# Performance work log

Measured on AMD Instinct MI355X. Metric: run time of the kernel, lower is better.

The kernel has to match this reference:

```python
import jax, jax.numpy as jnp
import numpy as np

N_WIRES = 9
N_QRAM_LAYERS = 3
N_QCLS_LAYERS = 5

X = jnp.array([[0, 1], [1, 0]], dtype=jnp.complex64)
CNOT = jnp.array([[1, 0, 0, 0], [0, 1, 0, 0], [0, 0, 0, 1], [0, 0, 1, 0]], dtype=jnp.complex64)


def _rx(t):
    c = jnp.cos(t / 2)
    s = jnp.sin(t / 2)
    # works for scalar t -> (2,2) or batched t [B] -> (B,2,2)
    return jnp.stack([jnp.stack([c + 0j, -1j * s], -1), jnp.stack([-1j * s, c + 0j], -1)], -2)


def _ry(t):
    c = jnp.cos(t / 2)
    s = jnp.sin(t / 2)
    return jnp.stack([jnp.stack([c, -s], -1), jnp.stack([s, c], -1)], -2).astype(jnp.complex64)


def _rz(t):
    e = jnp.exp(-0.5j * t)
    f = jnp.exp(0.5j * t)
    z = jnp.zeros_like(e)
    return jnp.stack([jnp.stack([e, z], -1), jnp.stack([z, f], -1)], -2)


def _rot(phi, theta, omega):
    # PennyLane Rot(phi, theta, omega) = RZ(omega) @ RY(theta) @ RZ(phi)
    return _rz(omega) @ _ry(theta) @ _rz(phi)


def _crz(t):
    e = jnp.exp(-0.5j * t)
    f = jnp.exp(0.5j * t)
    one = jnp.ones((), e.dtype)
    return jnp.diag(jnp.stack([one, one, e, f]))


def _crx(t):
    return jnp.eye(4, dtype=jnp.complex64).at[2:, 2:].set(_rx(t))


def apply_1q(state, U, w):
    # state: [B] + (2,)*N_WIRES ; wire w -> axis 1+w
    s = jnp.moveaxis(state, 1 + w, -1)
    if U.ndim == 3:  # per-sample gate (embedding)
        s = jnp.einsum('bij,b...j->b...i', U, s)
    else:
        s = jnp.einsum('ij,...j->...i', U, s)
    return jnp.moveaxis(s, -1, 1 + w)


def apply_2q(state, U, c, t):
    s = jnp.moveaxis(state, (1 + c, 1 + t), (-2, -1))
    shp = s.shape
    s = s.reshape(shp[:-2] + (4,))
    s = jnp.einsum('ij,...j->...i', U, s)
    return jnp.moveaxis(s.reshape(shp), (-2, -1), (1 + c, 1 + t))


def embed(state, adds):
    # AngleEmbedding: RX(adds[:, i]) on wire i
    for i in range(N_WIRES):
        state = apply_1q(state, _rx(adds[:, i]), i)
    return state


def entangle_block(state, p):
    # p: [36] = 4 params per wire-pair step
    j = 0
    for i in range(N_WIRES):
        ip = (i + 1) % N_WIRES
        state = apply_1q(state, _ry(p[j]), i)
        state = apply_1q(state, _ry(p[j + 1]), ip)
        state = apply_2q(state, CNOT, i, ip)
        state = apply_2q(state, _crz(p[j + 2]), i, ip)
        state = apply_1q(state, X, ip)
        state = apply_2q(state, _crx(p[j + 3]), i, ip)
        j += 4
    return state


def sel_layer(state, w, r):
    # one StronglyEntanglingLayers layer: Rot on each wire, then CNOT ring of range r
    for i in range(N_WIRES):
        state = apply_1q(state, _rot(w[i, 0], w[i, 1], w[i, 2]), i)
    for i in range(N_WIRES):
        state = apply_2q(state, CNOT, i, (i + r) % N_WIRES)
    return state


def circuit(adds, params, weights, params2):
    B = adds.shape[0]
    state = jnp.zeros((B,) + (2,) * N_WIRES, jnp.complex64)
    state = state.at[(slice(None),) + (0,) * N_WIRES].set(1.0)
    state = embed(state, adds)
    for l in range(N_QRAM_LAYERS):
        state = entangle_block(state, params[l * 36:(l + 1) * 36])
    for l in range(N_QRAM_LAYERS):
        r = (l % (N_WIRES - 1)) + 1  # PennyLane default ranges
        state = sel_layer(state, weights[l], r)
    for l in range(N_QCLS_LAYERS):
        state = entangle_block(state, params2[l * 36:(l + 1) * 36])
    probs = jnp.abs(state) ** 2
    p = probs.reshape(B, 2, -1).sum(-1)  # marginal over wire 0
    return p[:, 0] - p[:, 1]  # <PauliZ(0)>


def setup_inputs() -> dict:
    key = jax.random.key(0)
    k1, k2, k3, k4 = jax.random.split(key, 4)
    B = 8192
    return {
        'adds': jax.random.normal(k1, (B, N_WIRES), dtype=jnp.float32),
        'params': jax.random.normal(k2, (N_QRAM_LAYERS * 36,), dtype=jnp.float32),
        'weights': jax.random.normal(k3, (N_QRAM_LAYERS, N_WIRES, N_QRAM_LAYERS), dtype=jnp.float32),
        'params2': jax.random.normal(k4, (N_QCLS_LAYERS * 36,), dtype=jnp.float32),
    }


def reference(adds, params, weights, params2):
    return circuit(adds, params, weights, params2)
```

## Files before the change

### kernel.cpp

```cpp
#include <hip/hip_runtime.h>

#define NQ 9
#define NS 512
#define M2 1024
#define NSIMB 512

#define ENT_H_BASE 0
#define ROT_BASE   1024
#define ROT3_BASE  1240
#define M0123_BASE 1624
#define M78_BASE   5720
#define COEF_FLOATS 6744

typedef __attribute__((ext_vector_type(8))) short bf16x8;
typedef __attribute__((ext_vector_type(4))) float f32x4;

__device__ inline unsigned short f2bf(float f){
  unsigned int u = __float_as_uint(f);
  u += 0x7fffu + ((u >> 16) & 1u);
  return (unsigned short)(u >> 16);
}


template<int LM>
__device__ inline float lxor(float v){
  if constexpr (LM == 1)
    return __int_as_float(__builtin_amdgcn_mov_dpp(__float_as_int(v), 0xB1, 0xF, 0xF, true));
  else if constexpr (LM == 2)
    return __int_as_float(__builtin_amdgcn_mov_dpp(__float_as_int(v), 0x4E, 0xF, 0xF, true));
  else if constexpr (LM == 3)
    return __int_as_float(__builtin_amdgcn_mov_dpp(__float_as_int(v), 0x1B, 0xF, 0xF, true));
  else if constexpr (LM < 32)
    return __int_as_float(__builtin_amdgcn_ds_swizzle(__float_as_int(v), (LM<<10)|0x1F));
  else
    return __shfl_xor(v, LM);
}

template<int CM, int TM>
__device__ inline void step_swz(float& ax, float& ay, int lane, const float* g){
  float tx = lxor<TM>(ax),      ty = lxor<TM>(ay);
  float cx = lxor<CM>(ax),      cy = lxor<CM>(ay);
  float bx = lxor<(CM^TM)>(ax), by = lxor<(CM^TM)>(ay);
  int p = ((lane & CM) ? 2 : 0) | ((lane & TM) ? 1 : 0);
  float4 hx = *(const float4*)(g + p*4);
  float4 hy = *(const float4*)(g + 16 + p*4);
  float ox = ax, oy = ay;
  ax = hx.x*ox - hy.x*oy + hx.y*tx - hy.y*ty
     + hx.z*cx - hy.z*cy + hx.w*bx - hy.w*by;
  ay = hx.x*oy + hy.x*ox + hx.y*ty + hy.y*tx
     + hx.z*cy + hy.z*cx + hx.w*by + hy.w*bx;
}

__device__ inline void mrg16(float& ax, float& ay, int i, float2* xb, const float* Mt){
  xb[i] = make_float2(ax, ay);
  __syncthreads();
  int p = (i >> 5) & 15;
  const float* Mr = Mt + p*32;
  int base = i & 31;
  float s0x=0.f,s0y=0.f,s1x=0.f,s1y=0.f;
  #pragma unroll
  for (int q = 0; q < 16; q += 2){
    float2 v0 = xb[(q<<5)|base];
    float2 v1 = xb[((q+1)<<5)|base];
    float m0x = Mr[q*2],   m0y = Mr[q*2+1];
    float m1x = Mr[q*2+2], m1y = Mr[q*2+3];
    s0x += m0x*v0.x - m0y*v0.y;  s0y += m0x*v0.y + m0y*v0.x;
    s1x += m1x*v1.x - m1y*v1.y;  s1y += m1x*v1.y + m1y*v1.x;
  }
  ax = s0x + s1x; ay = s0y + s1y;
}

__device__ inline void mrg8_78(float& ax, float& ay, int i, float2* xb, const float* Mt){
  xb[i] = make_float2(ax, ay);
  __syncthreads();
  int p = (((i>>1)&1)<<2) | ((i&1)<<1) | ((i>>8)&1);
  const float* Mr = Mt + p*16;
  int ib = i & 0x0FC;
  float s0x=0.f,s0y=0.f,s1x=0.f,s1y=0.f;
  #pragma unroll
  for (int q = 0; q < 8; q += 2){
    int j0 = ib | ((q>>2)<<1) | ((q>>1)&1);
    float2 v0 = xb[j0];
    float2 v1 = xb[j0 | 0x100];
    float m0x = Mr[q*2],   m0y = Mr[q*2+1];
    float m1x = Mr[q*2+2], m1y = Mr[q*2+3];
    s0x += m0x*v0.x - m0y*v0.y;  s0y += m0x*v0.y + m0y*v0.x;
    s1x += m1x*v1.x - m1y*v1.y;  s1y += m1x*v1.y + m1y*v1.x;
  }
  ax = s0x + s1x; ay = s0y + s1y;
}

__device__ inline void rot3R(float& ax, float& ay, int i, float2* xb, const float* Mt){
  xb[i] = make_float2(ax, ay);
  __syncthreads();
  int p = i >> 6;
  const float* Mr = Mt + p*16;
  int base = i & 63;
  float s0x=0.f,s0y=0.f,s1x=0.f,s1y=0.f;
  #pragma unroll
  for (int q = 0; q < 8; q += 2){
    float2 v0 = xb[(q<<6)|base];
    float2 v1 = xb[((q+1)<<6)|base];
    float m0x = Mr[q*2],   m0y = Mr[q*2+1];
    float m1x = Mr[q*2+2], m1y = Mr[q*2+3];
    s0x += m0x*v0.x - m0y*v0.y;  s0y += m0x*v0.y + m0y*v0.x;
    s1x += m1x*v1.x - m1y*v1.y;  s1y += m1x*v1.y + m1y*v1.x;
  }
  ax = s0x + s1x; ay = s0y + s1y;
}

template<int LM>
__device__ inline void rot_swz(float& ax, float& ay, int lane, const float* u){
  float px = lxor<LM>(ax), py = lxor<LM>(ay);
  float4 uu = *(const float4*)(u + ((lane & LM) ? 4 : 0));
  float nx = uu.x*ax - uu.y*ay + uu.z*px - uu.w*py;
  float ny = uu.x*ay + uu.y*ax + uu.z*py + uu.w*px;
  ax = nx; ay = ny;
}

template<int I = 3>
__device__ inline void sel_lane_rots(float& ax, float& ay, int lane, const float* ub){
  rot_swz<(1<<(8-I))>(ax, ay, lane, ub + I*8);
  if constexpr (I < 8) sel_lane_rots<I+1>(ax, ay, lane, ub);
}

__device__ inline void ring_rt(float& ax, float& ay, int i, float2* buf, int R){
  buf[i] = make_float2(ax, ay);
  __syncthreads();
  int s = i;
  for (int k = 8; k >= 0; --k){
    int bc = 8 - k;
    int it = k + R; if (it >= 9) it -= 9;
    int bt = 8 - it;
    s ^= ((s >> bc) & 1) << bt;
  }
  float2 v = buf[s];
  ax = v.x; ay = v.y;
}

__device__ inline void entM(float& ax, float& ay, int i, int lane,
                            float2* bA, float2* bB, const float* scoef, int blk){
  mrg16(ax, ay, i, bA, scoef + M0123_BASE + blk*512);
  step_swz<32,16>(ax, ay, lane, scoef + ENT_H_BASE + (blk*4+0)*32);
  step_swz<16, 8>(ax, ay, lane, scoef + ENT_H_BASE + (blk*4+1)*32);
  step_swz< 8, 4>(ax, ay, lane, scoef + ENT_H_BASE + (blk*4+2)*32);
  step_swz< 4, 2>(ax, ay, lane, scoef + ENT_H_BASE + (blk*4+3)*32);
  mrg8_78(ax, ay, i, bB, scoef + M78_BASE + blk*128);
}


__global__ __launch_bounds__(512) void sim_prep(const float* __restrict__ params,
                                                const float* __restrict__ weights,
                                                const float* __restrict__ params2,
                                                const float* __restrict__ adds,
                                                unsigned short* __restrict__ A2,
                                                unsigned short* __restrict__ cT,
                                                float* __restrict__ out, int B){
  int tid = threadIdx.x;

  if (blockIdx.x >= NSIMB){
    int gid = (blockIdx.x - NSIMB) * 512 + tid;
    int b = gid >> 6;
    int lane = gid & 63;
    if (b < B){
      const float* ab = adds + b * NQ;
      float cw[NQ], sw[NQ];
      #pragma unroll
      for (int w = 0; w < NQ; ++w)
        __sincosf(0.5f * ab[w], &sw[w], &cw[w]);
      float p6 = 1.f;
      #pragma unroll
      for (int w = 0; w < 6; ++w)
        p6 *= ((lane >> (5 - w)) & 1) ? sw[w] : cw[w];
      union { unsigned short u[8]; uint4 v; } pk;
      #pragma unroll
      for (int j = 0; j < 8; ++j){
        float p = p6 * (((j>>2)&1) ? sw[6] : cw[6])
                     * (((j>>1)&1) ? sw[7] : cw[7])
                     * (( j    &1) ? sw[8] : cw[8]);
        pk.u[j] = f2bf(p);
      }
      *(uint4*)(cT + (size_t)b * NS + lane*8) = pk.v;
    }
    if (gid < B) out[gid] = 0.f;
    return;
  }

  __shared__ float2 ebuf[1024];
  __shared__ float scoef[COEF_FLOATS];
  float2* ebufA = ebuf;
  float2* ebufB = ebuf + 512;
  float* graw = (float*)ebuf;

  if (tid < 72){
    int blk = tid / 9, I = tid % 9;
    const float* p = (blk < 3) ? params + blk*36 : params2 + (blk-3)*36;
    float s0,c0,s1,c1,s2,c2,s3,c3;
    __sincosf(0.5f*p[4*I+0], &s0, &c0);
    __sincosf(0.5f*p[4*I+1], &s1, &c1);
    __sincosf(0.5f*p[4*I+2], &s2, &c2);
    __sincosf(0.5f*p[4*I+3], &s3, &c3);
    float m[4][4] = {
      { c0*c1, -c0*s1, -s0*c1,  s0*s1},
      { c0*s1,  c0*c1, -s0*s1, -s0*c1},
      { s0*c1, -s0*s1,  c0*c1, -c0*s1},
      { s0*s1,  s0*c1,  c0*s1,  c0*c1}};
    float gx[4][4], gy[4][4];
    #pragma unroll
    for (int q = 0; q < 4; ++q){
      gx[0][q] = m[1][q];  gy[0][q] = 0.f;
      gx[1][q] = m[0][q];  gy[1][q] = 0.f;
      gx[2][q] =  c3*c2*m[2][q] - s3*s2*m[3][q];
      gy[2][q] =  c3*s2*m[2][q] - s3*c2*m[3][q];
      gx[3][q] =  s3*s2*m[2][q] + c3*c2*m[3][q];
      gy[3][q] = -(s3*c2*m[2][q] + c3*s2*m[3][q]);
    }
    if (I >= 3 && I <= 6){
      float* dst = scoef + ENT_H_BASE + (blk*4 + (I-3))*32;
      #pragma unroll
      for (int pp = 0; pp < 4; ++pp)
        #pragma unroll
        for (int d = 0; d < 4; ++d){
          dst[pp*4+d]    = gx[pp][pp^d];
          dst[16+pp*4+d] = gy[pp][pp^d];
        }
    } else {
      float* dst = (I < 3) ? graw + (blk*3 + I)*32
                           : graw + 768 + (blk*2 + (I-7))*32;
      #pragma unroll
      for (int pp = 0; pp < 4; ++pp)
        #pragma unroll
        for (int q = 0; q < 4; ++q){
          dst[(pp*4+q)*2]   = gx[pp][q];
          dst[(pp*4+q)*2+1] = gy[pp][q];
        }
    }
  } else if (tid < 99){
    int r = tid - 72;
    int l = r / 9, i = r % 9;
    const float* w = weights + l*27 + 3*i;
    float phi = w[0], th = w[1], om = w[2];
    float sT,cT,sA,cA,sB,cB;
    __sincosf(0.5f*th, &sT, &cT);
    __sincosf(0.5f*(phi+om), &sA, &cA);
    __sincosf(0.5f*(om-phi), &sB, &cB);
    float* dst = scoef + ROT_BASE + r*8;
    dst[0] =  cA*cT;  dst[1] = -sA*cT;
    dst[2] = -cB*sT;  dst[3] =  sB*sT;
    dst[4] =  cA*cT;  dst[5] =  sA*cT;
    dst[6] =  cB*sT;  dst[7] =  sB*sT;
  } else if (tid < 123){
    int idx = tid - 99;
    int l = idx >> 3, p = idx & 7;
    float e0x[3], e0y[3], e1x[3], e1y[3];
    #pragma unroll
    for (int w = 0; w < 3; ++w){
      const float* wp = weights + l*27 + 3*w;
      float phi = wp[0], th = wp[1], om = wp[2];
      float sT,cT,sA,cA,sB,cB;
      __sincosf(0.5f*th, &sT, &cT);
      __sincosf(0.5f*(phi+om), &sA, &cA);
      __sincosf(0.5f*(om-phi), &sB, &cB);
      int pw = (p >> (2 - w)) & 1;
      if (pw == 0){ e0x[w] =  cA*cT; e0y[w] = -sA*cT; e1x[w] = -cB*sT; e1y[w] =  sB*sT; }
      else        { e0x[w] =  cB*sT; e0y[w] =  sB*sT; e1x[w] =  cA*cT; e1y[w] =  sA*cT; }
    }
    float* dst = scoef + ROT3_BASE + l*128 + p*16;
    #pragma unroll
    for (int q = 0; q < 8; ++q){
      float rx = 1.f, ry = 0.f;
      #pragma unroll
      for (int w = 0; w < 3; ++w){
        int qw = (q >> (2 - w)) & 1;
        float fx = qw ? e1x[w] : e0x[w];
        float fy = qw ? e1y[w] : e0y[w];
        float nx = rx*fx - ry*fy;
        float ny = rx*fy + ry*fx;
        rx = nx; ry = ny;
      }
      dst[q*2]   = rx;
      dst[q*2+1] = ry;
    }
  }
  __syncthreads();

  {
    int blk = tid >> 6;
    const float* G0 = graw + (blk*3+0)*32;
    const float* G1 = graw + (blk*3+1)*32;
    const float* G2 = graw + (blk*3+2)*32;
    int e4 = (tid & 63) * 4;
    #pragma unroll
    for (int k = 0; k < 4; ++k){
      int e = e4 + k;
      int p = e >> 4, q = e & 15;
      int a=(p>>3)&1, b=(p>>2)&1, c=(p>>1)&1, d=p&1;
      int ee=(q>>3)&1, f=(q>>2)&1, g=(q>>1)&1, h=q&1;
      float sx = 0.f, sy = 0.f;
      #pragma unroll
      for (int m = 0; m < 2; ++m)
        #pragma unroll
        for (int n = 0; n < 2; ++n){
          const float* z2 = G2 + ((c*2+d)*4 + (n*2+h))*2;
          const float* z1 = G1 + ((b*2+n)*4 + (m*2+g))*2;
          const float* z0 = G0 + ((a*2+m)*4 + (ee*2+f))*2;
          float ux = z2[0]*z1[0] - z2[1]*z1[1];
          float uy = z2[0]*z1[1] + z2[1]*z1[0];
          float vx = ux*z0[0] - uy*z0[1];
          float vy = ux*z0[1] + uy*z0[0];
          sx += vx; sy += vy;
        }
      scoef[M0123_BASE + blk*512 + (p*16+q)*2]   = sx;
      scoef[M0123_BASE + blk*512 + (p*16+q)*2+1] = sy;
    }
    const float* G7 = graw + 768 + (blk*2+0)*32;
    const float* G8 = graw + 768 + (blk*2+1)*32;
    int e = tid & 63;
    int p = e >> 3, q = e & 7;
    int a=(p>>2)&1, b=(p>>1)&1, c=p&1;
    int d=(q>>2)&1, ei=(q>>1)&1, f=q&1;
    float sx = 0.f, sy = 0.f;
    #pragma unroll
    for (int m = 0; m < 2; ++m){
      const float* z8 = G8 + ((b*2+c)*4 + (m*2+f))*2;
      const float* z7 = G7 + ((a*2+m)*4 + (d*2+ei))*2;
      sx += z8[0]*z7[0] - z8[1]*z7[1];
      sy += z8[0]*z7[1] + z8[1]*z7[0];
    }
    scoef[M78_BASE + blk*128 + (p*8+q)*2]   = sx;
    scoef[M78_BASE + blk*128 + (p*8+q)*2+1] = sy;
  }
  __syncthreads();

  int i = tid, lane = tid & 63;
  int col = blockIdx.x;
  float ax, ay;
  int pc = __popc((unsigned)col) & 3;
  float prx = (pc==0) ? 1.f : (pc==2 ? -1.f : 0.f);
  float pry = (pc==3) ? 1.f : (pc==1 ? -1.f : 0.f);
  ax = (i == col) ? prx : 0.f;
  ay = (i == col) ? pry : 0.f;

  #pragma unroll 1
  for (int blk = 0; blk < 3; ++blk)
    entM(ax, ay, i, lane, ebufA, ebufB, scoef, blk);
  #pragma unroll 1
  for (int L = 0; L < 3; ++L){
    rot3R(ax, ay, i, ebufA, scoef + ROT3_BASE + L*128);
    sel_lane_rots<3>(ax, ay, lane, scoef + ROT_BASE + L*72);
    ring_rt(ax, ay, i, ebufB, L + 1);
  }
  #pragma unroll 1
  for (int blk = 3; blk < 8; ++blk)
    entM(ax, ay, i, lane, ebufA, ebufB, scoef, blk);

  int c = col >> 3, sub = col & 7;
  size_t base = (size_t)c * 1024;
  A2[(base + i)*8 + sub]       = f2bf(ax);
  A2[(base + 512 + i)*8 + sub] = f2bf(ay);
}

__global__ __launch_bounds__(256) void gemm_out(const unsigned short* __restrict__ A2,
                                                const unsigned short* __restrict__ cT,
                                                float* __restrict__ out){
  int bx = blockIdx.x;
  int by = blockIdx.y;
  int tid = threadIdx.x;
  int wave = tid >> 6, lane = tid & 63;
  int wy = wave >> 1, wx = wave & 1;
  int lane15 = lane & 15, quad = lane >> 4;
  int rowBase = by*128 + wy*64;
  int colBase = bx*128 + wx*64;
  const bf16x8* Ap8 = (const bf16x8*)A2;
  const short* Bp = (const short*)cT;

  f32x4 acc[4][4];
  #pragma unroll
  for (int i = 0; i < 4; ++i)
    #pragma unroll
    for (int j = 0; j < 4; ++j)
      acc[i][j] = (f32x4){0.f, 0.f, 0.f, 0.f};

  #pragma unroll 4
  for (int k0 = 0; k0 < NS; k0 += 32){
    bf16x8 a[4], b[4];
    int c = (k0 >> 3) + quad;
    #pragma unroll
    for (int mi = 0; mi < 4; ++mi)
      a[mi] = Ap8[(size_t)c*1024 + rowBase + mi*16 + lane15];
    #pragma unroll
    for (int ni = 0; ni < 4; ++ni)
      b[ni] = *(const bf16x8*)(Bp + (size_t)(colBase + ni*16 + lane15)*NS + k0 + quad*8);
    #pragma unroll
    for (int mi = 0; mi < 4; ++mi)
      #pragma unroll
      for (int ni = 0; ni < 4; ++ni)
        acc[mi][ni] = __builtin_amdgcn_mfma_f32_16x16x32_bf16(a[mi], b[ni], acc[mi][ni], 0, 0, 0);
  }

  float sign = (by & 2) ? -1.f : 1.f;
  #pragma unroll
  for (int ni = 0; ni < 4; ++ni){
    float cs = 0.f;
    #pragma unroll
    for (int mi = 0; mi < 4; ++mi)
      #pragma unroll
      for (int r = 0; r < 4; ++r)
        cs += acc[mi][ni][r] * acc[mi][ni][r];
    cs += __shfl_xor(cs, 16);
    cs += __shfl_xor(cs, 32);
    if (quad == 0)
      atomicAdd(out + colBase + ni*16 + lane15, sign * cs);
  }
}

extern "C" void kernel_launch(void* const* d_in, const int* in_sizes, int n_in,
                              void* d_out, int out_size, void* d_ws, size_t ws_size,
                              hipStream_t stream) {
  const float* adds    = (const float*)d_in[0];
  const float* params  = (const float*)d_in[1];
  const float* weights = (const float*)d_in[2];
  const float* params2 = (const float*)d_in[3];
  float* out = (float*)d_out;
  int B = in_sizes[0] / NQ;

  unsigned short* A2 = (unsigned short*)d_ws;
  unsigned short* cT = A2 + (size_t)M2 * NS;

  int prepBlocks = (B * 64 + 511) / 512;
  hipLaunchKernelGGL(sim_prep, dim3(NSIMB + prepBlocks), dim3(512), 0, stream,
                     params, weights, params2, adds, A2, cT, out, B);
  hipLaunchKernelGGL(gemm_out, dim3(B / 128, 8), dim3(256), 0, stream, A2, cT, out);
}
```

Measured before the change: 113.8 us.

## Fuse selector layer rotations into 16x16 merged matrices and permute-on-write

The selector layers' 3-wire rotation matmul and the first lane rotation are now precomputed into a single 16x16 complex matrix per layer, applied with the existing mrg16 routine. The ring CNOT permutation is folded into the shared-memory write index through a precomputed lookup table, which removes a separate store/sync/load pass per layer. The GEMM kernel is also changed to 512 threads with 8 waves, each computing a 64x32 tile, which halves per-wave accumulator registers. The fused step does more multiply-adds per element, and shared memory usage grows.

```diff
diff --git a/kernel.cpp b/kernel.cpp
--- a/kernel.cpp
+++ b/kernel.cpp
@@ -8,9 +8,10 @@
 #define ENT_H_BASE 0
 #define ROT_BASE   1024
 #define ROT3_BASE  1240
-#define M0123_BASE 1624
-#define M78_BASE   5720
-#define COEF_FLOATS 6744
+#define ROT16_BASE 1624
+#define M0123_BASE 3160
+#define M78_BASE   7256
+#define COEF_FLOATS 8280
 
 typedef __attribute__((ext_vector_type(8))) short bf16x8;
 typedef __attribute__((ext_vector_type(4))) float f32x4;
@@ -51,8 +52,9 @@
      + hx.z*cy + hy.z*cx + hx.w*by + hy.w*bx;
 }
 
-__device__ inline void mrg16(float& ax, float& ay, int i, float2* xb, const float* Mt){
-  xb[i] = make_float2(ax, ay);
+__device__ inline void mrg16(float& ax, float& ay, int i, int wi, float2* xb,
+                             const float* Mt){
+  xb[wi] = make_float2(ax, ay);
   __syncthreads();
   int p = (i >> 5) & 15;
   const float* Mr = Mt + p*32;
@@ -90,25 +92,6 @@
   ax = s0x + s1x; ay = s0y + s1y;
 }
 
-__device__ inline void rot3R(float& ax, float& ay, int i, float2* xb, const float* Mt){
-  xb[i] = make_float2(ax, ay);
-  __syncthreads();
-  int p = i >> 6;
-  const float* Mr = Mt + p*16;
-  int base = i & 63;
-  float s0x=0.f,s0y=0.f,s1x=0.f,s1y=0.f;
-  #pragma unroll
-  for (int q = 0; q < 8; q += 2){
-    float2 v0 = xb[(q<<6)|base];
-    float2 v1 = xb[((q+1)<<6)|base];
-    float m0x = Mr[q*2],   m0y = Mr[q*2+1];
-    float m1x = Mr[q*2+2], m1y = Mr[q*2+3];
-    s0x += m0x*v0.x - m0y*v0.y;  s0y += m0x*v0.y + m0y*v0.x;
-    s1x += m1x*v1.x - m1y*v1.y;  s1y += m1x*v1.y + m1y*v1.x;
-  }
-  ax = s0x + s1x; ay = s0y + s1y;
-}
-
 template<int LM>
 __device__ inline void rot_swz(float& ax, float& ay, int lane, const float* u){
   float px = lxor<LM>(ax), py = lxor<LM>(ay);
@@ -118,34 +101,20 @@
   ax = nx; ay = ny;
 }
 
-template<int I = 3>
+template<int I = 4>
 __device__ inline void sel_lane_rots(float& ax, float& ay, int lane, const float* ub){
   rot_swz<(1<<(8-I))>(ax, ay, lane, ub + I*8);
   if constexpr (I < 8) sel_lane_rots<I+1>(ax, ay, lane, ub);
 }
 
-__device__ inline void ring_rt(float& ax, float& ay, int i, float2* buf, int R){
-  buf[i] = make_float2(ax, ay);
-  __syncthreads();
-  int s = i;
-  for (int k = 8; k >= 0; --k){
-    int bc = 8 - k;
-    int it = k + R; if (it >= 9) it -= 9;
-    int bt = 8 - it;
-    s ^= ((s >> bc) & 1) << bt;
-  }
-  float2 v = buf[s];
-  ax = v.x; ay = v.y;
-}
-
-__device__ inline void entM(float& ax, float& ay, int i, int lane,
-                            float2* bA, float2* bB, const float* scoef, int blk){
-  mrg16(ax, ay, i, bA, scoef + M0123_BASE + blk*512);
+__device__ inline void entM(float& ax, float& ay, int i, int wi, int lane,
+                            float2* bX, float2* bY, const float* scoef, int blk){
+  mrg16(ax, ay, i, wi, bX, scoef + M0123_BASE + blk*512);
   step_swz<32,16>(ax, ay, lane, scoef + ENT_H_BASE + (blk*4+0)*32);
   step_swz<16, 8>(ax, ay, lane, scoef + ENT_H_BASE + (blk*4+1)*32);
   step_swz< 8, 4>(ax, ay, lane, scoef + ENT_H_BASE + (blk*4+2)*32);
   step_swz< 4, 2>(ax, ay, lane, scoef + ENT_H_BASE + (blk*4+3)*32);
-  mrg8_78(ax, ay, i, bB, scoef + M78_BASE + blk*128);
+  mrg8_78(ax, ay, i, bY, scoef + M78_BASE + blk*128);
 }
 
 
@@ -188,6 +157,7 @@
 
   __shared__ float2 ebuf[1024];
   __shared__ float scoef[COEF_FLOATS];
+  __shared__ unsigned short slut[3][512];
   float2* ebufA = ebuf;
   float2* ebufB = ebuf + 512;
   float* graw = (float*)ebuf;
@@ -329,11 +299,37 @@
     }
     scoef[M78_BASE + blk*128 + (p*8+q)*2]   = sx;
     scoef[M78_BASE + blk*128 + (p*8+q)*2+1] = sy;
+
+    for (int e2 = tid; e2 < 768; e2 += 512){
+      int l = e2 >> 8, pq = e2 & 255;
+      int pp = pq >> 4, qq = pq & 15;
+      const float* R3 = scoef + ROT3_BASE + l*128 + (pp>>1)*16 + (qq>>1)*2;
+      const float* U = scoef + ROT_BASE + (l*9+3)*8;
+      int pb = pp & 1, qb = qq & 1;
+      float ux, uy;
+      if (pb == 0){ if (qb == 0){ ux=U[0]; uy=U[1]; } else { ux=U[2]; uy=U[3]; } }
+      else        { if (qb == 1){ ux=U[4]; uy=U[5]; } else { ux=U[6]; uy=U[7]; } }
+      float rx = R3[0], ry = R3[1];
+      scoef[ROT16_BASE + l*512 + pp*32 + qq*2]   = rx*ux - ry*uy;
+      scoef[ROT16_BASE + l*512 + pp*32 + qq*2+1] = rx*uy + ry*ux;
+    }
+
+    for (int R = 1; R <= 3; ++R){
+      int s = tid;
+      for (int k = 8; k >= 0; --k){
+        int bc = 8 - k;
+        int it = k + R; if (it >= 9) it -= 9;
+        int bt = 8 - it;
+        s ^= ((s >> bc) & 1) << bt;
+      }
+      slut[R-1][s] = (unsigned short)tid;
+    }
   }
   __syncthreads();
 
   int i = tid, lane = tid & 63;
   int col = blockIdx.x;
+  int w1 = slut[0][i], w2 = slut[1][i], w3 = slut[2][i];
   float ax, ay;
   int pc = __popc((unsigned)col) & 3;
   float prx = (pc==0) ? 1.f : (pc==2 ? -1.f : 0.f);
@@ -343,16 +339,19 @@
 
   #pragma unroll 1
   for (int blk = 0; blk < 3; ++blk)
-    entM(ax, ay, i, lane, ebufA, ebufB, scoef, blk);
+    entM(ax, ay, i, i, lane, ebufA, ebufB, scoef, blk);
+
+  mrg16(ax, ay, i, i,  ebufA, scoef + ROT16_BASE + 0*512);
+  sel_lane_rots<4>(ax, ay, lane, scoef + ROT_BASE + 0*72);
+  mrg16(ax, ay, i, w1, ebufB, scoef + ROT16_BASE + 1*512);
+  sel_lane_rots<4>(ax, ay, lane, scoef + ROT_BASE + 1*72);
+  mrg16(ax, ay, i, w2, ebufA, scoef + ROT16_BASE + 2*512);
+  sel_lane_rots<4>(ax, ay, lane, scoef + ROT_BASE + 2*72);
+
+  entM(ax, ay, i, w3, lane, ebufB, ebufA, scoef, 3);
   #pragma unroll 1
-  for (int L = 0; L < 3; ++L){
-    rot3R(ax, ay, i, ebufA, scoef + ROT3_BASE + L*128);
-    sel_lane_rots<3>(ax, ay, lane, scoef + ROT_BASE + L*72);
-    ring_rt(ax, ay, i, ebufB, L + 1);
-  }
-  #pragma unroll 1
-  for (int blk = 3; blk < 8; ++blk)
-    entM(ax, ay, i, lane, ebufA, ebufB, scoef, blk);
+  for (int blk = 4; blk < 8; ++blk)
+    entM(ax, ay, i, i, lane, ebufB, ebufA, scoef, blk);
 
   int c = col >> 3, sub = col & 7;
   size_t base = (size_t)c * 1024;
@@ -360,47 +359,47 @@
   A2[(base + 512 + i)*8 + sub] = f2bf(ay);
 }
 
-__global__ __launch_bounds__(256) void gemm_out(const unsigned short* __restrict__ A2,
+__global__ __launch_bounds__(512) void gemm_out(const unsigned short* __restrict__ A2,
                                                 const unsigned short* __restrict__ cT,
                                                 float* __restrict__ out){
   int bx = blockIdx.x;
   int by = blockIdx.y;
   int tid = threadIdx.x;
   int wave = tid >> 6, lane = tid & 63;
-  int wy = wave >> 1, wx = wave & 1;
+  int wy = wave >> 2, wx = wave & 3;
   int lane15 = lane & 15, quad = lane >> 4;
   int rowBase = by*128 + wy*64;
-  int colBase = bx*128 + wx*64;
+  int colBase = bx*128 + wx*32;
   const bf16x8* Ap8 = (const bf16x8*)A2;
   const short* Bp = (const short*)cT;
 
-  f32x4 acc[4][4];
+  f32x4 acc[4][2];
   #pragma unroll
   for (int i = 0; i < 4; ++i)
     #pragma unroll
-    for (int j = 0; j < 4; ++j)
+    for (int j = 0; j < 2; ++j)
       acc[i][j] = (f32x4){0.f, 0.f, 0.f, 0.f};
 
   #pragma unroll 4
   for (int k0 = 0; k0 < NS; k0 += 32){
-    bf16x8 a[4], b[4];
+    bf16x8 a[4], b[2];
     int c = (k0 >> 3) + quad;
     #pragma unroll
     for (int mi = 0; mi < 4; ++mi)
       a[mi] = Ap8[(size_t)c*1024 + rowBase + mi*16 + lane15];
     #pragma unroll
-    for (int ni = 0; ni < 4; ++ni)
+    for (int ni = 0; ni < 2; ++ni)
       b[ni] = *(const bf16x8*)(Bp + (size_t)(colBase + ni*16 + lane15)*NS + k0 + quad*8);
     #pragma unroll
     for (int mi = 0; mi < 4; ++mi)
       #pragma unroll
-      for (int ni = 0; ni < 4; ++ni)
+      for (int ni = 0; ni < 2; ++ni)
         acc[mi][ni] = __builtin_amdgcn_mfma_f32_16x16x32_bf16(a[mi], b[ni], acc[mi][ni], 0, 0, 0);
   }
 
   float sign = (by & 2) ? -1.f : 1.f;
   #pragma unroll
-  for (int ni = 0; ni < 4; ++ni){
+  for (int ni = 0; ni < 2; ++ni){
     float cs = 0.f;
     #pragma unroll
     for (int mi = 0; mi < 4; ++mi)
@@ -430,5 +429,5 @@
   int prepBlocks = (B * 64 + 511) / 512;
   hipLaunchKernelGGL(sim_prep, dim3(NSIMB + prepBlocks), dim3(512), 0, stream,
                      params, weights, params2, adds, A2, cT, out, B);
-  hipLaunchKernelGGL(gemm_out, dim3(B / 128, 8), dim3(256), 0, stream, A2, cT, out);
-}
+  hipLaunchKernelGGL(gemm_out, dim3(B / 128, 8), dim3(512), 0, stream, A2, cT, out);
+}
```

After: 116.7 us. 1.03x slower.
